# Kernel tuning notes

Measured on AMD Instinct MI355X. Metric: run time of the kernel, lower is better.

Reference implementation:

```python
import jax, jax.numpy as jnp
import numpy as np


def _ln(z, g, b, eps=1e-5):
    mu = z.mean(-1, keepdims=True)
    v = ((z - mu) ** 2).mean(-1, keepdims=True)
    return (z - mu) / jnp.sqrt(v + eps) * g + b


def _forward(x, C_prev, n_prev, m_prev, ln_in_g, ln_in_b, wq, bq, wk, bk, wv, bv, wi, bi, wf, bf, wo, bo, rd_w1, rd_b1, rd_g, rd_be, rd_w2, rd_b2, ssm_log_lam, ssm_log_b, ssm_c, ssm_log_d, ssm_log_step, ssm_vol_gate, ssm_alpha, ssm_ln_g, ssm_ln_b, ln_mem_g, ln_mem_b):
    B, S, F = x.shape
    D = wq.shape[0]
    sqd = jnp.sqrt(jnp.float32(D))
    w = max(1, int(S * 0.2))
    pad0 = jnp.zeros((B, 1, F), x.dtype)
    cs = jnp.concatenate([pad0, jnp.cumsum(x, 1)], 1)
    cs2 = jnp.concatenate([pad0, jnp.cumsum(x * x, 1)], 1)
    wsum = cs[:, w:] - cs[:, :-w]
    wsq = cs2[:, w:] - cs2[:, :-w]
    var = (wsq - wsum * wsum / w) / (w - 1)
    std = jnp.sqrt(jnp.clip(var, 0.0))
    vol = jnp.concatenate([jnp.broadcast_to(std[:, :1], (B, w - 1, F)), std], 1)
    sv = vol.mean(2, keepdims=True)
    sv = sv / (sv.mean(1, keepdims=True) + 1e-6)  # [B,S,1]
    # --- parallel gate computation ---
    xn = _ln(x, ln_in_g, ln_in_b)
    regime = jax.nn.softmax(jax.nn.gelu(_ln(xn @ rd_w1.T + rd_b1, rd_g, rd_be), approximate=False) @ rd_w2.T + rd_b2, axis=-1)
    q = xn @ wq.T + bq
    k = (xn @ wk.T + bk) / sqd
    v = xn @ wv.T + bv
    it = xn @ wi.T + bi  # [B,S,1]
    ft = xn @ wf.T + bf
    o = jax.nn.sigmoid(xn @ wo.T + bo)
    # --- stabilize_gates (running-max exponential stabilization) ---
    mp = jnp.clip(m_prev, -100.0, 100.0)[:, None, :]  # [B,1,1]
    m_t = jnp.maximum(ft, mp + ft)
    ig = jnp.exp(jnp.clip(it - m_t, -15.0, 15.0))
    fg = jnp.exp(jnp.clip(ft + mp - m_t, -15.0, 15.0))
    # --- store_key_value outer products + cumulative matrix memory ---
    kn = k / (jnp.linalg.norm(k, axis=2, keepdims=True) + 1e-12) * sqd
    vn = v / (jnp.linalg.norm(v, axis=2, keepdims=True) + 1e-6) * sqd
    upd = jnp.clip(ig, 0.0, 1.0)[..., None] * (vn[..., :, None] * kn[..., None, :])  # [B,S,D,D]
    f_cum = jnp.cumprod(fg, axis=1)  # [B,S,1]
    C_t = f_cum[..., None] * C_prev[:, None] + jnp.cumsum(upd, 1)
    # --- structured state-space mixing, vectorized over the D memory rows ---
    lam = -jnp.exp(ssm_log_lam)
    step = jnp.exp(ssm_log_step)
    a_disc = (2.0 + step * lam) / (2.0 - step * lam)  # bilinear discretization
    b_disc = step * (1.0 + a_disc) * jnp.exp(ssm_log_b)[:, 0] / 2.0
    xr = C_t.transpose(0, 2, 1, 3).reshape(B * D, S, D)  # rows folded into batch
    volr = jnp.broadcast_to(sv[:, None, :, 0], (B, D, S)).reshape(B * D, S)
    u = xr.mean(-1)  # [BD,S], per-step scalar drive
    vgate = jax.nn.sigmoid(ssm_vol_gate)
    def stepf(h, inp):
        u_t, vol_t = inp
        h = a_disc[None] * h + b_disc[None] * u_t[:, None]
        h = _ln(h, ssm_ln_g, ssm_ln_b)
        h = h / (1.0 + vgate[None] * vol_t[:, None])
        return h, h
    h0 = jnp.zeros((B * D, D), x.dtype)
    _, hs = jax.lax.scan(stepf, h0, (u.T, volr.T))  # [S,BD,D]
    yscal = jnp.einsum('sbn,n->bs', hs, ssm_c[0])  # [BD,S]
    y = yscal[..., None] + jnp.exp(ssm_log_d) * xr
    alpha = jax.nn.sigmoid(ssm_alpha)
    mixed = alpha * xr + (1.0 - alpha) * y
    C_mixed = mixed.reshape(B, D, S, D).transpose(0, 2, 1, 3)
    mf = regime[:, :, 0:1][..., None]  # regime-aware mixing factor
    C_t = C_mixed * mf + C_t * (1.0 - mf)
    C_t = C_t / (jnp.linalg.norm(C_t.reshape(B, S, D * D), axis=-1)[..., None, None] + 1e-6) * sqd
    # --- mLSTM readout (stabilizer_threshold = 1.0) ---
    n_t = f_cum * n_prev[:, None, :] + jnp.cumsum(ig * k, 1)
    h_til = jnp.einsum('bsij,bsj->bsi', C_t, q)
    denom = jnp.maximum(jnp.abs(jnp.sum(n_t * q, -1, keepdims=True)), 1.0)
    return o * _ln(h_til / denom, ln_mem_g, ln_mem_b)


def setup_inputs() -> dict:
    key = jax.random.key(0)
    ks = jax.random.split(key, 12)
    B, S, F, D = 8, 512, 32, 64
    sF, sD = 1.0 / np.sqrt(F), 1.0 / np.sqrt(D)
    n = lambda k, sh, s=1.0: jax.random.normal(k, sh, jnp.float32) * s
    return dict(
        x=n(ks[0], (B, S, F)),
        C_prev=jnp.zeros((B, D, D), jnp.float32),
        n_prev=jnp.zeros((B, D), jnp.float32),
        m_prev=jnp.zeros((B, 1), jnp.float32),
        ln_in_g=jnp.ones((F,), jnp.float32), ln_in_b=jnp.zeros((F,), jnp.float32),
        wq=n(ks[1], (D, F), sF), bq=jnp.zeros((D,), jnp.float32),
        wk=n(ks[2], (D, F), sF), bk=jnp.zeros((D,), jnp.float32),
        wv=n(ks[3], (D, F), sF), bv=jnp.zeros((D,), jnp.float32),
        wi=n(ks[4], (1, F), sF), bi=jnp.zeros((1,), jnp.float32),
        wf=n(ks[5], (1, F), sF), bf=jnp.ones((1,), jnp.float32),
        wo=n(ks[6], (D, F), sF), bo=jnp.zeros((D,), jnp.float32),
        rd_w1=n(ks[7], (D, F), sF), rd_b1=jnp.zeros((D,), jnp.float32),
        rd_g=jnp.ones((D,), jnp.float32), rd_be=jnp.zeros((D,), jnp.float32),
        rd_w2=n(ks[8], (4, D), sD), rd_b2=jnp.zeros((4,), jnp.float32),
        ssm_log_lam=jnp.linspace(np.log(0.001), np.log(0.1), D).astype(jnp.float32),
        ssm_log_b=jax.random.uniform(ks[9], (D, 1), jnp.float32, -0.5, 0.5),
        ssm_c=n(ks[10], (1, D), sD),
        ssm_log_d=jnp.zeros((1,), jnp.float32),
        ssm_log_step=jnp.float32(np.log(0.001)),
        ssm_vol_gate=jnp.ones((D,), jnp.float32),
        ssm_alpha=jnp.float32(0.7),
        ssm_ln_g=jnp.ones((D,), jnp.float32), ssm_ln_b=jnp.zeros((D,), jnp.float32),
        ln_mem_g=jnp.ones((D,), jnp.float32), ln_mem_b=jnp.zeros((D,), jnp.float32),
    )


def reference(x, C_prev, n_prev, m_prev, ln_in_g, ln_in_b, wq, bq, wk, bk, wv, bv, wi, bi, wf, bf, wo, bo, rd_w1, rd_b1, rd_g, rd_be, rd_w2, rd_b2, ssm_log_lam, ssm_log_b, ssm_c, ssm_log_d, ssm_log_step, ssm_vol_gate, ssm_alpha, ssm_ln_g, ssm_ln_b, ln_mem_g, ln_mem_b):
    return _forward(x, C_prev, n_prev, m_prev, ln_in_g, ln_in_b, wq, bq, wk, bk, wv, bv, wi, bi, wf, bf, wo, bo, rd_w1, rd_b1, rd_g, rd_be, rd_w2, rd_b2, ssm_log_lam, ssm_log_b, ssm_c, ssm_log_d, ssm_log_step, ssm_vol_gate, ssm_alpha, ssm_ln_g, ssm_ln_b, ln_mem_g, ln_mem_b)
```

## Files before the change

### kernel.cpp

```cpp
#include <hip/hip_runtime.h>
#include <math.h>

#define BB 8
#define SS 512
#define FF 32
#define DD 64
#define WVOL 102

template<int CTRL, int RM, bool BC>
__device__ __forceinline__ float updpp(float oldv, float x) {
  return __int_as_float(__builtin_amdgcn_update_dpp(
      __float_as_int(oldv), __float_as_int(x), CTRL, RM, 0xF, BC));
}
__device__ __forceinline__ float rlane(float v, int l) {
  return __int_as_float(__builtin_amdgcn_readlane(__float_as_int(v), l));
}
__device__ __forceinline__ float dsum64(float x) {
  x += updpp<0x111, 0xF, true>(0.f, x);
  x += updpp<0x112, 0xF, true>(0.f, x);
  x += updpp<0x114, 0xF, true>(0.f, x);
  x += updpp<0x118, 0xF, true>(0.f, x);
  x += updpp<0x142, 0xF, true>(0.f, x);
  x += updpp<0x143, 0xF, true>(0.f, x);
  return rlane(x, 63);
}
__device__ __forceinline__ float dsum32(float x) {
  x += updpp<0x111, 0xF, true>(0.f, x);
  x += updpp<0x112, 0xF, true>(0.f, x);
  x += updpp<0x114, 0xF, true>(0.f, x);
  x += updpp<0x118, 0xF, true>(0.f, x);
  x += updpp<0x142, 0xF, true>(0.f, x);
  return rlane(x, 31);
}
__device__ __forceinline__ float dscan_add(float x) {
  x += updpp<0x111, 0xF, true>(0.f, x);
  x += updpp<0x112, 0xF, true>(0.f, x);
  x += updpp<0x114, 0xF, true>(0.f, x);
  x += updpp<0x118, 0xF, true>(0.f, x);
  x += updpp<0x142, 0xA, true>(0.f, x);
  x += updpp<0x143, 0xC, true>(0.f, x);
  return x;
}
__device__ __forceinline__ float dscan_mul(float x) {
  x *= updpp<0x111, 0xF, false>(1.f, x);
  x *= updpp<0x112, 0xF, false>(1.f, x);
  x *= updpp<0x114, 0xF, false>(1.f, x);
  x *= updpp<0x118, 0xF, false>(1.f, x);
  x *= updpp<0x142, 0xA, false>(1.f, x);
  x *= updpp<0x143, 0xC, false>(1.f, x);
  return x;
}

__global__ void k_vol_std(const float* __restrict__ x, float* __restrict__ svraw) {
  int b = blockIdx.x; int s = WVOL - 1 + blockIdx.y;
  int lane = threadIdx.x; int f = lane & 31; int half = lane >> 5;
  const float* xb = x + (size_t)(b * SS) * FF + f;
  float wsum = 0.f, wsq = 0.f;
  int t0 = s - WVOL + 1 + half;
#pragma unroll 17
  for (int k = 0; k < WVOL / 2; ++k) {
    float xv = xb[(t0 + 2 * k) * FF];
    wsum += xv; wsq = fmaf(xv, xv, wsq);
  }
  wsum += __shfl_xor(wsum, 32); wsq += __shfl_xor(wsq, 32);
  float var = (wsq - wsum * wsum * (1.f / WVOL)) * (1.f / (WVOL - 1));
  float sd = sqrtf(fmaxf(var, 0.f));
  float m = dsum64(sd) * 0.5f * (1.f / FF);
  if (lane == 0) svraw[b * SS + s] = m;
}

__global__ void k_vol_norm(const float* __restrict__ svraw, float* __restrict__ sv) {
  int b = blockIdx.x; int tid = threadIdx.x;
  float m0 = svraw[b * SS + WVOL - 1];
  float val = (tid < WVOL - 1) ? m0 : svraw[b * SS + tid];
  float ws = dsum64(val);
  __shared__ float part[8];
  if ((tid & 63) == 0) part[tid >> 6] = ws;
  __syncthreads();
  float tot = 0.f;
#pragma unroll
  for (int i = 0; i < 8; ++i) tot += part[i];
  float inv = 1.f / (tot * (1.f / SS) + 1e-6f);
  sv[b * SS + tid] = val * inv;
}

__global__ void k_proj(const float* __restrict__ x, const float* __restrict__ m_prev,
                       const float* __restrict__ ln_in_g, const float* __restrict__ ln_in_b,
                       const float* __restrict__ wq, const float* __restrict__ bq,
                       const float* __restrict__ wk, const float* __restrict__ bk,
                       const float* __restrict__ wv, const float* __restrict__ bv,
                       const float* __restrict__ wi, const float* __restrict__ bi,
                       const float* __restrict__ wf, const float* __restrict__ bf,
                       const float* __restrict__ wo, const float* __restrict__ bo,
                       const float* __restrict__ rd_w1, const float* __restrict__ rd_b1,
                       const float* __restrict__ rd_g, const float* __restrict__ rd_be,
                       const float* __restrict__ rd_w2, const float* __restrict__ rd_b2,
                       float* __restrict__ qo, float* __restrict__ kno, float* __restrict__ vno,
                       float* __restrict__ iko, float* __restrict__ oo,
                       float* __restrict__ knT, float* __restrict__ vnT,
                       float* __restrict__ cg_a, float* __restrict__ fg_a,
                       float* __restrict__ mf_a, float* __restrict__ cks_a,
                       float* __restrict__ qsum_a) {
  int bs = blockIdx.x; int b = bs / SS; int s = bs % SS;
  int lane = threadIdx.x;
  __shared__ float xs[FF];
  float xv = (lane < FF) ? x[bs * FF + lane] : 0.f;
  float s1x = dsum32(xv);
  float s2x = dsum32(xv * xv);
  if (lane < FF) {
    float mu = s1x * (1.f / FF);
    float var = s2x * (1.f / FF) - mu * mu;
    xs[lane] = (xv - mu) * rsqrtf(var + 1e-5f) * ln_in_g[lane] + ln_in_b[lane];
  }
  __syncthreads();
  int d = lane;
  float aq = bq[d], ak = bk[d], av = bv[d], ao = bo[d], at = rd_b1[d];
#pragma unroll
  for (int f = 0; f < FF; ++f) {
    float xf = xs[f];
    aq = fmaf(xf, wq[d * FF + f], aq);
    ak = fmaf(xf, wk[d * FF + f], ak);
    av = fmaf(xf, wv[d * FF + f], av);
    ao = fmaf(xf, wo[d * FF + f], ao);
    at = fmaf(xf, rd_w1[d * FF + f], at);
  }
  float pit = (lane < FF) ? xs[lane] * wi[lane] : 0.f;
  float pft = (lane < FF) ? xs[lane] * wf[lane] : 0.f;
  float itv = dsum32(pit) + bi[0];
  float ftv = dsum32(pft) + bf[0];
  float s1 = dsum64(at), s2 = dsum64(at * at);
  float mu = s1 * (1.f / DD);
  float var = s2 * (1.f / DD) - mu * mu;
  float tn = (at - mu) * rsqrtf(var + 1e-5f) * rd_g[d] + rd_be[d];
  float ge = 0.5f * tn * (1.f + erff(tn * 0.70710678118654752f));
  float l0 = dsum64(ge * rd_w2[0 * DD + d]) + rd_b2[0];
  float l1 = dsum64(ge * rd_w2[1 * DD + d]) + rd_b2[1];
  float l2 = dsum64(ge * rd_w2[2 * DD + d]) + rd_b2[2];
  float l3 = dsum64(ge * rd_w2[3 * DD + d]) + rd_b2[3];
  float mx = fmaxf(fmaxf(l0, l1), fmaxf(l2, l3));
  float e0 = expf(l0 - mx), e1 = expf(l1 - mx), e2 = expf(l2 - mx), e3 = expf(l3 - mx);
  float mfv = e0 / (e0 + e1 + e2 + e3);
  float kd = ak * 0.125f;
  float kk = dsum64(kd * kd);
  float knd = kd * (8.f / (sqrtf(kk) + 1e-12f));
  float vv = dsum64(av * av);
  float vnd = av * (8.f / (sqrtf(vv) + 1e-6f));
  float ksum = dsum64(knd);
  float qsum = dsum64(aq);
  float mp = fminf(fmaxf(m_prev[b], -100.f), 100.f);
  float mt = fmaxf(ftv, mp + ftv);
  float ig = expf(fminf(fmaxf(itv - mt, -15.f), 15.f));
  float fg = expf(fminf(fmaxf(ftv + mp - mt, -15.f), 15.f));
  float cg = fminf(ig, 1.f);
  qo[bs * DD + d] = aq;
  kno[bs * DD + d] = knd;
  vno[bs * DD + d] = vnd;
  iko[bs * DD + d] = ig * kd;
  oo[bs * DD + d] = 1.f / (1.f + expf(-ao));
  knT[(b * DD + d) * SS + s] = knd;
  vnT[(b * DD + d) * SS + s] = vnd;
  if (lane == 0) {
    cg_a[bs] = cg; fg_a[bs] = fg; mf_a[bs] = mfv;
    cks_a[bs] = cg * ksum; qsum_a[bs] = qsum;
  }
}

__global__ void k_zc(const float* __restrict__ kno, const float* __restrict__ vno,
                     const float* __restrict__ Cp, const float* __restrict__ cg_a,
                     float* __restrict__ zc) {
  int bs = blockIdx.x; int b = bs / SS;
  int i = threadIdx.x;
  __shared__ float ks[DD];
  ks[i] = kno[bs * DD + i];
  __syncthreads();
  float acc = 0.f;
  const float* cr = Cp + (b * DD + i) * DD;
#pragma unroll
  for (int j = 0; j < DD; ++j) acc = fmaf(cr[j], ks[j], acc);
  float z = dsum64(vno[bs * DD + i] * acc);
  if (i == 0) zc[bs] = cg_a[bs] * z;
}

__global__ void k_main(const float* __restrict__ qo, const float* __restrict__ kno,
                       const float* __restrict__ vno,
                       const float* __restrict__ knT, const float* __restrict__ vnT,
                       const float* __restrict__ cg_a,
                       float* __restrict__ p2, float* __restrict__ rho) {
  int bs = blockIdx.x; int b = bs / SS; int s = bs % SS;
  int lane = threadIdx.x;
  __shared__ float w[64];
  const float* qrow = qo + bs * DD;
  const float* krow = kno + bs * DD;
  const float* vrow = vno + bs * DD;
  float pacc = 0.f, rp = 0.f;
  int sT = s & ~63;
  for (int T = 0; T < sT; T += 64) {
    int t = T + lane;
    float A = 0.f, KK = 0.f, VV = 0.f;
#pragma unroll 8
    for (int j = 0; j < DD; ++j) {
      float kt = knT[(b * DD + j) * SS + t];
      float vt = vnT[(b * DD + j) * SS + t];
      A = fmaf(kt, qrow[j], A);
      KK = fmaf(kt, krow[j], KK);
      VV = fmaf(vt, vrow[j], VV);
    }
    float cgt = cg_a[b * SS + t];
    w[lane] = cgt * A;
    rp = fmaf(2.f * cgt, KK * VV, rp);
    __syncthreads();
#pragma unroll 8
    for (int tl = 0; tl < 64; ++tl)
      pacc = fmaf(w[tl], vno[(b * SS + T + tl) * DD + lane], pacc);
    __syncthreads();
  }
  {
    int T = sT; int t = T + lane;
    float A = 0.f, KK = 0.f, VV = 0.f;
#pragma unroll 8
    for (int j = 0; j < DD; ++j) {
      float kt = knT[(b * DD + j) * SS + t];
      float vt = vnT[(b * DD + j) * SS + t];
      A = fmaf(kt, qrow[j], A);
      KK = fmaf(kt, krow[j], KK);
      VV = fmaf(vt, vrow[j], VV);
    }
    float cgt = cg_a[b * SS + t];
    w[lane] = (t <= s) ? cgt * A : 0.f;
    float wr = (t < s) ? 2.f : (t == s ? 1.f : 0.f);
    rp = fmaf(wr * cgt, KK * VV, rp);
    __syncthreads();
    int tmax = s - sT;
    for (int tl = 0; tl <= tmax; ++tl)
      pacc = fmaf(w[tl], vno[(b * SS + T + tl) * DD + lane], pacc);
  }
  p2[bs * DD + lane] = pacc;
  float rr = dsum64(rp);
  if (lane == 0) rho[bs] = cg_a[bs] * rr;
}

__global__ void k_scalar_scan(const float* __restrict__ fg_a, const float* __restrict__ zc,
                              const float* __restrict__ rho, const float* __restrict__ Cp,
                              float* __restrict__ fcum, float* __restrict__ cpd,
                              float* __restrict__ sn2, float* __restrict__ cpr,
                              float* __restrict__ cpn2) {
  int b = blockIdx.x; int lane = threadIdx.x;
  float rs = 0.f, r2 = 0.f;
  const float* cr = Cp + (b * DD + lane) * DD;
#pragma unroll
  for (int j = 0; j < DD; ++j) { float c = cr[j]; rs += c; r2 = fmaf(c, c, r2); }
  cpr[b * DD + lane] = rs;
  float tot2 = dsum64(r2);
  if (lane == 0) cpn2[b] = tot2;
  float cf = 1.f, cz = 0.f, crr = 0.f;
  for (int c = 0; c < 8; ++c) {
    int bs = b * SS + c * 64 + lane;
    float f = dscan_mul(fg_a[bs]) * cf;
    float z = dscan_add(zc[bs]) + cz;
    float r = dscan_add(rho[bs]) + crr;
    fcum[bs] = f; cpd[bs] = z; sn2[bs] = r;
    cf = rlane(f, 63); cz = rlane(z, 63); crr = rlane(r, 63);
  }
}

__global__ void k_scan_vec(const float* __restrict__ ik, const float* __restrict__ vno,
                           const float* __restrict__ cks_a,
                           float* __restrict__ nacc, float* __restrict__ racc) {
  int b = blockIdx.x;
  int w = threadIdx.x >> 6, d = threadIdx.x & 63;
  __shared__ float T[2][8][DD];
  float na = 0.f, ra = 0.f;
  int s0 = w * 64;
  for (int t = 0; t < 64; ++t) {
    int bs = b * SS + s0 + t;
    na += ik[bs * DD + d];
    ra = fmaf(cks_a[bs], vno[bs * DD + d], ra);
  }
  T[0][w][d] = na; T[1][w][d] = ra;
  __syncthreads();
  na = 0.f; ra = 0.f;
  for (int w2 = 0; w2 < w; ++w2) { na += T[0][w2][d]; ra += T[1][w2][d]; }
  for (int t = 0; t < 64; ++t) {
    int bs = b * SS + s0 + t;
    na += ik[bs * DD + d];
    ra = fmaf(cks_a[bs], vno[bs * DD + d], ra);
    nacc[bs * DD + d] = na;
    racc[bs * DD + d] = ra;
  }
}

__global__ void k_ssm(const float* __restrict__ fcum, const float* __restrict__ racc,
                      const float* __restrict__ cpr, const float* __restrict__ sv,
                      const float* __restrict__ log_lam, const float* __restrict__ log_b,
                      const float* __restrict__ cvec,
                      const float* __restrict__ log_step, const float* __restrict__ vol_gate,
                      const float* __restrict__ ln_g, const float* __restrict__ ln_b,
                      float* __restrict__ ys) {
  int blk = blockIdx.x; int b = blk >> 6; int i = blk & 63;
  int n = threadIdx.x;
  float st = expf(log_step[0]);
  float lam = -expf(log_lam[n]);
  float ad = (2.f + st * lam) / (2.f - st * lam);
  float bd = st * (1.f + ad) * expf(log_b[n]) * 0.5f;
  float vg = 1.f / (1.f + expf(-vol_gate[n]));
  float g = ln_g[n], be = ln_b[n], cn = cvec[n];
  float cprv = cpr[b * DD + i];
  float u[8], w[8];
#pragma unroll
  for (int c = 0; c < 8; ++c) {
    int s = c * 64 + n; int bs = b * SS + s;
    u[c] = fmaf(fcum[bs], cprv, racc[(size_t)bs * DD + i]) * (1.f / DD);
    w[c] = sv[bs];
  }
  float h = 0.f;
#pragma unroll
  for (int c = 0; c < 8; ++c) {
    float yreg = 0.f;
    for (int t = 0; t < 64; ++t) {
      float uu = rlane(u[c], t);
      float vv = rlane(w[c], t);
      float ht = fmaf(ad, h, bd * uu);
      float p1 = ht, p2 = ht * ht;
      p1 += updpp<0x111, 0xF, true>(0.f, p1); p2 += updpp<0x111, 0xF, true>(0.f, p2);
      p1 += updpp<0x112, 0xF, true>(0.f, p1); p2 += updpp<0x112, 0xF, true>(0.f, p2);
      p1 += updpp<0x114, 0xF, true>(0.f, p1); p2 += updpp<0x114, 0xF, true>(0.f, p2);
      p1 += updpp<0x118, 0xF, true>(0.f, p1); p2 += updpp<0x118, 0xF, true>(0.f, p2);
      p1 += updpp<0x142, 0xF, true>(0.f, p1); p2 += updpp<0x142, 0xF, true>(0.f, p2);
      p1 += updpp<0x143, 0xF, true>(0.f, p1); p2 += updpp<0x143, 0xF, true>(0.f, p2);
      float s1 = rlane(p1, 63), s2 = rlane(p2, 63);
      float mu = s1 * (1.f / DD);
      float var = fmaxf(s2 * (1.f / DD) - mu * mu, 0.f);
      float hn = fmaf((ht - mu) * rsqrtf(var + 1e-5f), g, be);
      float hv = __fdividef(hn, fmaf(vg, vv, 1.f));
      h = hv;
      float y = cn * hv;
      y += updpp<0x111, 0xF, true>(0.f, y);
      y += updpp<0x112, 0xF, true>(0.f, y);
      y += updpp<0x114, 0xF, true>(0.f, y);
      y += updpp<0x118, 0xF, true>(0.f, y);
      y += updpp<0x142, 0xF, true>(0.f, y);
      y += updpp<0x143, 0xF, true>(0.f, y);
      float su = rlane(y, 63);
      yreg = (n == t) ? su : yreg;
    }
    ys[(size_t)(b * SS + c * 64 + n) * DD + i] = yreg;
  }
}

__global__ void k_final(const float* __restrict__ qo, const float* __restrict__ oo,
                        const float* __restrict__ p2, const float* __restrict__ racc,
                        const float* __restrict__ nacc, const float* __restrict__ ys,
                        const float* __restrict__ Cp, const float* __restrict__ cpr,
                        const float* __restrict__ cpn2,
                        const float* __restrict__ fcum, const float* __restrict__ cpd,
                        const float* __restrict__ sn2,
                        const float* __restrict__ mf_a, const float* __restrict__ qsum_a,
                        const float* __restrict__ n_prev,
                        const float* __restrict__ ssm_log_d, const float* __restrict__ ssm_alpha,
                        const float* __restrict__ ln_mem_g, const float* __restrict__ ln_mem_b,
                        float* __restrict__ out) {
  int bs = blockIdx.x; int b = bs / SS;
  int i = threadIdx.x;
  __shared__ float qv[DD];
  float qi = qo[bs * DD + i];
  qv[i] = qi;
  __syncthreads();
  float P1 = 0.f;
  const float* cr = Cp + (b * DD + i) * DD;
#pragma unroll
  for (int j = 0; j < DD; ++j) P1 = fmaf(cr[j], qv[j], P1);
  float fc = fcum[bs];
  float p = fmaf(fc, P1, p2[bs * DD + i]);
  float r = fmaf(fc, cpr[b * DD + i], racc[bs * DD + i]);
  float R2 = fc * fc * cpn2[b] + 2.f * fc * cpd[bs] + sn2[bs];
  float al = 1.f / (1.f + expf(-ssm_alpha[0]));
  float kap = al + (1.f - al) * expf(ssm_log_d[0]);
  float mfv = mf_a[bs];
  float beta = 1.f + mfv * (kap - 1.f);
  float gam = mfv * (1.f - al);
  float y = ys[bs * DD + i];
  float syr = dsum64(y * r);
  float sy2 = dsum64(y * y);
  float nrm2 = fmaxf(beta * beta * R2 + 2.f * beta * gam * syr + gam * gam * (float)DD * sy2, 0.f);
  float scale = 8.f / (sqrtf(nrm2) + 1e-6f);
  float nt = fmaf(fc, n_prev[b * DD + i], nacc[bs * DD + i]);
  float ndp = dsum64(nt * qi);
  float denom = fmaxf(fabsf(ndp), 1.f);
  float hh = scale * (fmaf(beta, p, gam * y * qsum_a[bs])) / denom;
  float s1 = dsum64(hh), s2 = dsum64(hh * hh);
  float mu = s1 * (1.f / DD);
  float var = fmaxf(s2 * (1.f / DD) - mu * mu, 0.f);
  float o = (hh - mu) * rsqrtf(var + 1e-5f) * ln_mem_g[i] + ln_mem_b[i];
  out[bs * DD + i] = oo[bs * DD + i] * o;
}

extern "C" void kernel_launch(void* const* d_in, const int* in_sizes, int n_in,
                              void* d_out, int out_size, void* d_ws, size_t ws_size,
                              hipStream_t stream) {
  const float* x        = (const float*)d_in[0];
  const float* C_prev   = (const float*)d_in[1];
  const float* n_prev   = (const float*)d_in[2];
  const float* m_prev   = (const float*)d_in[3];
  const float* ln_in_g  = (const float*)d_in[4];
  const float* ln_in_b  = (const float*)d_in[5];
  const float* wq = (const float*)d_in[6];  const float* bq = (const float*)d_in[7];
  const float* wk = (const float*)d_in[8];  const float* bk = (const float*)d_in[9];
  const float* wv = (const float*)d_in[10]; const float* bv = (const float*)d_in[11];
  const float* wi = (const float*)d_in[12]; const float* bi = (const float*)d_in[13];
  const float* wf = (const float*)d_in[14]; const float* bf = (const float*)d_in[15];
  const float* wo = (const float*)d_in[16]; const float* bo = (const float*)d_in[17];
  const float* rd_w1 = (const float*)d_in[18]; const float* rd_b1 = (const float*)d_in[19];
  const float* rd_g  = (const float*)d_in[20]; const float* rd_be = (const float*)d_in[21];
  const float* rd_w2 = (const float*)d_in[22]; const float* rd_b2 = (const float*)d_in[23];
  const float* ssm_log_lam  = (const float*)d_in[24];
  const float* ssm_log_b    = (const float*)d_in[25];
  const float* ssm_c        = (const float*)d_in[26];
  const float* ssm_log_d    = (const float*)d_in[27];
  const float* ssm_log_step = (const float*)d_in[28];
  const float* ssm_vol_gate = (const float*)d_in[29];
  const float* ssm_alpha    = (const float*)d_in[30];
  const float* ssm_ln_g     = (const float*)d_in[31];
  const float* ssm_ln_b     = (const float*)d_in[32];
  const float* ln_mem_g     = (const float*)d_in[33];
  const float* ln_mem_b     = (const float*)d_in[34];
  float* out = (float*)d_out;

  float* W = (float*)d_ws;
  size_t o0 = 0;
  const size_t BS = (size_t)BB * SS, BSD = BS * DD;
  float* sv    = W + o0; o0 += BS;
  float* svraw = W + o0; o0 += BS;
  float* qo   = W + o0; o0 += BSD;
  float* kno  = W + o0; o0 += BSD;
  float* vno  = W + o0; o0 += BSD;
  float* iko  = W + o0; o0 += BSD;
  float* oo   = W + o0; o0 += BSD;
  float* knT  = W + o0; o0 += BSD;
  float* vnT  = W + o0; o0 += BSD;
  float* p2   = W + o0; o0 += BSD;
  float* racc = W + o0; o0 += BSD;
  float* nacc = W + o0; o0 += BSD;
  float* ysb  = W + o0; o0 += BSD;
  float* cg_a = W + o0; o0 += BS;
  float* fg_a = W + o0; o0 += BS;
  float* mf_a = W + o0; o0 += BS;
  float* cks  = W + o0; o0 += BS;
  float* qsum = W + o0; o0 += BS;
  float* zc   = W + o0; o0 += BS;
  float* fcum = W + o0; o0 += BS;
  float* cpd  = W + o0; o0 += BS;
  float* rho  = W + o0; o0 += BS;
  float* sn2  = W + o0; o0 += BS;
  float* cpr  = W + o0; o0 += (size_t)BB * DD;
  float* cpn2 = W + o0; o0 += BB;

  hipLaunchKernelGGL(k_vol_std, dim3(BB, SS - WVOL + 1), dim3(64), 0, stream, x, svraw);
  hipLaunchKernelGGL(k_vol_norm, dim3(BB), dim3(SS), 0, stream, svraw, sv);
  hipLaunchKernelGGL(k_proj, dim3(BB * SS), dim3(64), 0, stream,
                     x, m_prev, ln_in_g, ln_in_b, wq, bq, wk, bk, wv, bv, wi, bi,
                     wf, bf, wo, bo, rd_w1, rd_b1, rd_g, rd_be, rd_w2, rd_b2,
                     qo, kno, vno, iko, oo, knT, vnT, cg_a, fg_a, mf_a, cks, qsum);
  hipLaunchKernelGGL(k_zc, dim3(BB * SS), dim3(64), 0, stream, kno, vno, C_prev, cg_a, zc);
  hipLaunchKernelGGL(k_main, dim3(BB * SS), dim3(64), 0, stream,
                     qo, kno, vno, knT, vnT, cg_a, p2, rho);
  hipLaunchKernelGGL(k_scalar_scan, dim3(BB), dim3(64), 0, stream,
                     fg_a, zc, rho, C_prev, fcum, cpd, sn2, cpr, cpn2);
  hipLaunchKernelGGL(k_scan_vec, dim3(BB), dim3(512), 0, stream,
                     iko, vno, cks, nacc, racc);
  hipLaunchKernelGGL(k_ssm, dim3(BB * DD), dim3(64), 0, stream,
                     fcum, racc, cpr, sv, ssm_log_lam, ssm_log_b, ssm_c,
                     ssm_log_step, ssm_vol_gate, ssm_ln_g, ssm_ln_b, ysb);
  hipLaunchKernelGGL(k_final, dim3(BB * SS), dim3(64), 0, stream,
                     qo, oo, p2, racc, nacc, ysb, C_prev, cpr, cpn2, fcum, cpd, sn2,
                     mf_a, qsum, n_prev, ssm_log_d, ssm_alpha, ln_mem_g, ln_mem_b, out);
}
```

Baseline: 365.0 us.

## Fuse zc into projection, parallelize vector scan, streamline SSM recurrence

Moves the C_prev·k·v dot product from k_zc into k_proj and the volatility normalization into k_scalar_scan, which removes two launches and a reload of kno/vno. The single-block-per-batch vector scan becomes a two-pass chunked scan over 16-step chunks (k_csum plus k_scan_apply) spread across many blocks. The sequential SSM loop hoists the reciprocal of the volume gate off the reduction chain, uses hardware rcp and rsq intrinsics, and writes y transposed so each store is coalesced. k_final then reads y with a strided transposed access, and the approximate intrinsics may change rounding slightly.

```diff
diff --git a/kernel.cpp b/kernel.cpp
--- a/kernel.cpp
+++ b/kernel.cpp
@@ -6,6 +6,8 @@
 #define FF 32
 #define DD 64
 #define WVOL 102
+#define CH 16
+#define NCH (SS / CH)
 
 template<int CTRL, int RM, bool BC>
 __device__ __forceinline__ float updpp(float oldv, float x) {
@@ -69,22 +71,8 @@
   if (lane == 0) svraw[b * SS + s] = m;
 }
 
-__global__ void k_vol_norm(const float* __restrict__ svraw, float* __restrict__ sv) {
-  int b = blockIdx.x; int tid = threadIdx.x;
-  float m0 = svraw[b * SS + WVOL - 1];
-  float val = (tid < WVOL - 1) ? m0 : svraw[b * SS + tid];
-  float ws = dsum64(val);
-  __shared__ float part[8];
-  if ((tid & 63) == 0) part[tid >> 6] = ws;
-  __syncthreads();
-  float tot = 0.f;
-#pragma unroll
-  for (int i = 0; i < 8; ++i) tot += part[i];
-  float inv = 1.f / (tot * (1.f / SS) + 1e-6f);
-  sv[b * SS + tid] = val * inv;
-}
-
 __global__ void k_proj(const float* __restrict__ x, const float* __restrict__ m_prev,
+                       const float* __restrict__ Cp,
                        const float* __restrict__ ln_in_g, const float* __restrict__ ln_in_b,
                        const float* __restrict__ wq, const float* __restrict__ bq,
                        const float* __restrict__ wk, const float* __restrict__ bk,
@@ -100,10 +88,11 @@
                        float* __restrict__ knT, float* __restrict__ vnT,
                        float* __restrict__ cg_a, float* __restrict__ fg_a,
                        float* __restrict__ mf_a, float* __restrict__ cks_a,
-                       float* __restrict__ qsum_a) {
+                       float* __restrict__ qsum_a, float* __restrict__ zc) {
   int bs = blockIdx.x; int b = bs / SS; int s = bs % SS;
   int lane = threadIdx.x;
   __shared__ float xs[FF];
+  __shared__ float ks[DD];
   float xv = (lane < FF) ? x[bs * FF + lane] : 0.f;
   float s1x = dsum32(xv);
   float s2x = dsum32(xv * xv);
@@ -159,26 +148,18 @@
   oo[bs * DD + d] = 1.f / (1.f + expf(-ao));
   knT[(b * DD + d) * SS + s] = knd;
   vnT[(b * DD + d) * SS + s] = vnd;
+  ks[d] = knd;
+  __syncthreads();
+  float acc = 0.f;
+  const float* cr = Cp + (b * DD + d) * DD;
+#pragma unroll
+  for (int j = 0; j < DD; ++j) acc = fmaf(cr[j], ks[j], acc);
+  float z = dsum64(vnd * acc);
   if (lane == 0) {
     cg_a[bs] = cg; fg_a[bs] = fg; mf_a[bs] = mfv;
     cks_a[bs] = cg * ksum; qsum_a[bs] = qsum;
-  }
-}
-
-__global__ void k_zc(const float* __restrict__ kno, const float* __restrict__ vno,
-                     const float* __restrict__ Cp, const float* __restrict__ cg_a,
-                     float* __restrict__ zc) {
-  int bs = blockIdx.x; int b = bs / SS;
-  int i = threadIdx.x;
-  __shared__ float ks[DD];
-  ks[i] = kno[bs * DD + i];
-  __syncthreads();
-  float acc = 0.f;
-  const float* cr = Cp + (b * DD + i) * DD;
-#pragma unroll
-  for (int j = 0; j < DD; ++j) acc = fmaf(cr[j], ks[j], acc);
-  float z = dsum64(vno[bs * DD + i] * acc);
-  if (i == 0) zc[bs] = cg_a[bs] * z;
+    zc[bs] = cg * z;
+  }
 }
 
 __global__ void k_main(const float* __restrict__ qo, const float* __restrict__ kno,
@@ -241,9 +222,10 @@
 
 __global__ void k_scalar_scan(const float* __restrict__ fg_a, const float* __restrict__ zc,
                               const float* __restrict__ rho, const float* __restrict__ Cp,
+                              const float* __restrict__ svraw,
                               float* __restrict__ fcum, float* __restrict__ cpd,
                               float* __restrict__ sn2, float* __restrict__ cpr,
-                              float* __restrict__ cpn2) {
+                              float* __restrict__ cpn2, float* __restrict__ sv) {
   int b = blockIdx.x; int lane = threadIdx.x;
   float rs = 0.f, r2 = 0.f;
   const float* cr = Cp + (b * DD + lane) * DD;
@@ -252,6 +234,18 @@
   cpr[b * DD + lane] = rs;
   float tot2 = dsum64(r2);
   if (lane == 0) cpn2[b] = tot2;
+  float m0 = svraw[b * SS + WVOL - 1];
+  float vals[8]; float part = 0.f;
+#pragma unroll
+  for (int c = 0; c < 8; ++c) {
+    int idx = c * 64 + lane;
+    float v = (idx < WVOL - 1) ? m0 : svraw[b * SS + idx];
+    vals[c] = v; part += v;
+  }
+  float tot = dsum64(part);
+  float inv = 1.f / (tot * (1.f / SS) + 1e-6f);
+#pragma unroll
+  for (int c = 0; c < 8; ++c) sv[b * SS + c * 64 + lane] = vals[c] * inv;
   float cf = 1.f, cz = 0.f, crr = 0.f;
   for (int c = 0; c < 8; ++c) {
     int bs = b * SS + c * 64 + lane;
@@ -263,25 +257,32 @@
   }
 }
 
-__global__ void k_scan_vec(const float* __restrict__ ik, const float* __restrict__ vno,
-                           const float* __restrict__ cks_a,
-                           float* __restrict__ nacc, float* __restrict__ racc) {
-  int b = blockIdx.x;
-  int w = threadIdx.x >> 6, d = threadIdx.x & 63;
-  __shared__ float T[2][8][DD];
+__global__ void k_csum(const float* __restrict__ ik, const float* __restrict__ vno,
+                       const float* __restrict__ cks_a,
+                       float* __restrict__ csn, float* __restrict__ csr) {
+  int blk = blockIdx.x; int b = blk / NCH; int w = blk % NCH; int d = threadIdx.x;
   float na = 0.f, ra = 0.f;
-  int s0 = w * 64;
-  for (int t = 0; t < 64; ++t) {
-    int bs = b * SS + s0 + t;
+#pragma unroll
+  for (int t = 0; t < CH; ++t) {
+    int bs = b * SS + w * CH + t;
     na += ik[bs * DD + d];
     ra = fmaf(cks_a[bs], vno[bs * DD + d], ra);
   }
-  T[0][w][d] = na; T[1][w][d] = ra;
-  __syncthreads();
-  na = 0.f; ra = 0.f;
-  for (int w2 = 0; w2 < w; ++w2) { na += T[0][w2][d]; ra += T[1][w2][d]; }
-  for (int t = 0; t < 64; ++t) {
-    int bs = b * SS + s0 + t;
+  csn[blk * DD + d] = na; csr[blk * DD + d] = ra;
+}
+__global__ void k_scan_apply(const float* __restrict__ ik, const float* __restrict__ vno,
+                             const float* __restrict__ cks_a,
+                             const float* __restrict__ csn, const float* __restrict__ csr,
+                             float* __restrict__ nacc, float* __restrict__ racc) {
+  int blk = blockIdx.x; int b = blk / NCH; int w = blk % NCH; int d = threadIdx.x;
+  float na = 0.f, ra = 0.f;
+  for (int w2 = 0; w2 < w; ++w2) {
+    na += csn[(b * NCH + w2) * DD + d];
+    ra += csr[(b * NCH + w2) * DD + d];
+  }
+#pragma unroll
+  for (int t = 0; t < CH; ++t) {
+    int bs = b * SS + w * CH + t;
     na += ik[bs * DD + d];
     ra = fmaf(cks_a[bs], vno[bs * DD + d], ra);
     nacc[bs * DD + d] = na;
@@ -295,7 +296,7 @@
                       const float* __restrict__ cvec,
                       const float* __restrict__ log_step, const float* __restrict__ vol_gate,
                       const float* __restrict__ ln_g, const float* __restrict__ ln_b,
-                      float* __restrict__ ys) {
+                      float* __restrict__ ysT) {
   int blk = blockIdx.x; int b = blk >> 6; int i = blk & 63;
   int n = threadIdx.x;
   float st = expf(log_step[0]);
@@ -315,11 +316,15 @@
   float h = 0.f;
 #pragma unroll
   for (int c = 0; c < 8; ++c) {
-    float yreg = 0.f;
+    float yout = 0.f;
+#pragma unroll 4
     for (int t = 0; t < 64; ++t) {
       float uu = rlane(u[c], t);
       float vv = rlane(w[c], t);
-      float ht = fmaf(ad, h, bd * uu);
+      float bdu = bd * uu;
+      float rden = __builtin_amdgcn_rcpf(fmaf(vg, vv, 1.f));
+      float grden = g * rden, berden = be * rden;
+      float ht = fmaf(ad, h, bdu);
       float p1 = ht, p2 = ht * ht;
       p1 += updpp<0x111, 0xF, true>(0.f, p1); p2 += updpp<0x111, 0xF, true>(0.f, p2);
       p1 += updpp<0x112, 0xF, true>(0.f, p1); p2 += updpp<0x112, 0xF, true>(0.f, p2);
@@ -329,9 +334,10 @@
       p1 += updpp<0x143, 0xF, true>(0.f, p1); p2 += updpp<0x143, 0xF, true>(0.f, p2);
       float s1 = rlane(p1, 63), s2 = rlane(p2, 63);
       float mu = s1 * (1.f / DD);
-      float var = fmaxf(s2 * (1.f / DD) - mu * mu, 0.f);
-      float hn = fmaf((ht - mu) * rsqrtf(var + 1e-5f), g, be);
-      float hv = __fdividef(hn, fmaf(vg, vv, 1.f));
+      float r2m = fmaf(-mu, s1, s2);
+      float arg = fmaxf(fmaf(r2m, 1.f / DD, 1e-5f), 1e-5f);
+      float irs = __builtin_amdgcn_rsqf(arg);
+      float hv = fmaf((ht - mu) * grden, irs, berden);
       h = hv;
       float y = cn * hv;
       y += updpp<0x111, 0xF, true>(0.f, y);
@@ -341,15 +347,15 @@
       y += updpp<0x142, 0xF, true>(0.f, y);
       y += updpp<0x143, 0xF, true>(0.f, y);
       float su = rlane(y, 63);
-      yreg = (n == t) ? su : yreg;
+      yout = (n == t) ? su : yout;
     }
-    ys[(size_t)(b * SS + c * 64 + n) * DD + i] = yreg;
+    ysT[(size_t)(b * DD + i) * SS + c * 64 + n] = yout;
   }
 }
 
 __global__ void k_final(const float* __restrict__ qo, const float* __restrict__ oo,
                         const float* __restrict__ p2, const float* __restrict__ racc,
-                        const float* __restrict__ nacc, const float* __restrict__ ys,
+                        const float* __restrict__ nacc, const float* __restrict__ ysT,
                         const float* __restrict__ Cp, const float* __restrict__ cpr,
                         const float* __restrict__ cpn2,
                         const float* __restrict__ fcum, const float* __restrict__ cpd,
@@ -359,7 +365,7 @@
                         const float* __restrict__ ssm_log_d, const float* __restrict__ ssm_alpha,
                         const float* __restrict__ ln_mem_g, const float* __restrict__ ln_mem_b,
                         float* __restrict__ out) {
-  int bs = blockIdx.x; int b = bs / SS;
+  int bs = blockIdx.x; int b = bs / SS; int s = bs % SS;
   int i = threadIdx.x;
   __shared__ float qv[DD];
   float qi = qo[bs * DD + i];
@@ -378,7 +384,7 @@
   float mfv = mf_a[bs];
   float beta = 1.f + mfv * (kap - 1.f);
   float gam = mfv * (1.f - al);
-  float y = ys[bs * DD + i];
+  float y = ysT[(size_t)(b * DD + i) * SS + s];
   float syr = dsum64(y * r);
   float sy2 = dsum64(y * y);
   float nrm2 = fmaxf(beta * beta * R2 + 2.f * beta * gam * syr + gam * gam * (float)DD * sy2, 0.f);
@@ -440,7 +446,7 @@
   float* p2   = W + o0; o0 += BSD;
   float* racc = W + o0; o0 += BSD;
   float* nacc = W + o0; o0 += BSD;
-  float* ysb  = W + o0; o0 += BSD;
+  float* ysT  = W + o0; o0 += BSD;
   float* cg_a = W + o0; o0 += BS;
   float* fg_a = W + o0; o0 += BS;
   float* mf_a = W + o0; o0 += BS;
@@ -453,24 +459,26 @@
   float* sn2  = W + o0; o0 += BS;
   float* cpr  = W + o0; o0 += (size_t)BB * DD;
   float* cpn2 = W + o0; o0 += BB;
+  float* csn  = W + o0; o0 += (size_t)BB * NCH * DD;
+  float* csr  = W + o0; o0 += (size_t)BB * NCH * DD;
 
   hipLaunchKernelGGL(k_vol_std, dim3(BB, SS - WVOL + 1), dim3(64), 0, stream, x, svraw);
-  hipLaunchKernelGGL(k_vol_norm, dim3(BB), dim3(SS), 0, stream, svraw, sv);
   hipLaunchKernelGGL(k_proj, dim3(BB * SS), dim3(64), 0, stream,
-                     x, m_prev, ln_in_g, ln_in_b, wq, bq, wk, bk, wv, bv, wi, bi,
+                     x, m_prev, C_prev, ln_in_g, ln_in_b, wq, bq, wk, bk, wv, bv, wi, bi,
                      wf, bf, wo, bo, rd_w1, rd_b1, rd_g, rd_be, rd_w2, rd_b2,
-                     qo, kno, vno, iko, oo, knT, vnT, cg_a, fg_a, mf_a, cks, qsum);
-  hipLaunchKernelGGL(k_zc, dim3(BB * SS), dim3(64), 0, stream, kno, vno, C_prev, cg_a, zc);
+                     qo, kno, vno, iko, oo, knT, vnT, cg_a, fg_a, mf_a, cks, qsum, zc);
   hipLaunchKernelGGL(k_main, dim3(BB * SS), dim3(64), 0, stream,
                      qo, kno, vno, knT, vnT, cg_a, p2, rho);
   hipLaunchKernelGGL(k_scalar_scan, dim3(BB), dim3(64), 0, stream,
-                     fg_a, zc, rho, C_prev, fcum, cpd, sn2, cpr, cpn2);
-  hipLaunchKernelGGL(k_scan_vec, dim3(BB), dim3(512), 0, stream,
-                     iko, vno, cks, nacc, racc);
+                     fg_a, zc, rho, C_prev, svraw, fcum, cpd, sn2, cpr, cpn2, sv);
+  hipLaunchKernelGGL(k_csum, dim3(BB * NCH), dim3(64), 0, stream,
+                     iko, vno, cks, csn, csr);
+  hipLaunchKernelGGL(k_scan_apply, dim3(BB * NCH), dim3(64), 0, stream,
+                     iko, vno, cks, csn, csr, nacc, racc);
   hipLaunchKernelGGL(k_ssm, dim3(BB * DD), dim3(64), 0, stream,
                      fcum, racc, cpr, sv, ssm_log_lam, ssm_log_b, ssm_c,
-                     ssm_log_step, ssm_vol_gate, ssm_ln_g, ssm_ln_b, ysb);
+                     ssm_log_step, ssm_vol_gate, ssm_ln_g, ssm_ln_b, ysT);
   hipLaunchKernelGGL(k_final, dim3(BB * SS), dim3(64), 0, stream,
-                     qo, oo, p2, racc, nacc, ysb, C_prev, cpr, cpn2, fcum, cpd, sn2,
+                     qo, oo, p2, racc, nacc, ysT, C_prev, cpr, cpn2, fcum, cpd, sn2,
                      mf_a, qsum, n_prev, ssm_log_d, ssm_alpha, ln_mem_g, ln_mem_b, out);
 }
```

After: 332.3 us. 9.0% less time.
